# Kernel optimization log

Measured on AMD Instinct MI355X. Metric: run time of the kernel, lower is better.

## Reference

```python
import jax, jax.numpy as jnp
import numpy as np

N = 50000      # num nodes
E = 800000     # num edges (before self loops)
H = 2          # heads
C = 64         # out_channels (== in_dim, extra_layer=False)
L = 3          # n_layer
SLOPE = 0.2    # leaky_relu negative_slope


def setup_inputs() -> dict:
    key = jax.random.key(0)
    k1, k2, k3 = jax.random.split(key, 3)
    x = jax.random.normal(k1, (N, C), dtype=jnp.float32)
    edge_index = jax.random.randint(k2, (2, E), 0, N)
    att = jax.random.normal(k3, (L, H, C), dtype=jnp.float32) * 0.1  # glorot-ish scale
    bias = jnp.zeros((L, C), dtype=jnp.float32)
    return {"x": x, "edge_index": edge_index, "att": att, "bias": bias}


def _segment_softmax(alpha, dst, n):
    # alpha: [Etot, H], softmax over edges sharing the same destination node
    m = jax.ops.segment_max(alpha, dst, num_segments=n)          # [N, H]
    a = jnp.exp(alpha - m[dst])                                  # [Etot, H]
    s = jax.ops.segment_sum(a, dst, num_segments=n)              # [N, H]
    return a / (s[dst] + 1e-16)


def _gat_layer(x, src, dst, att_l, bias_l):
    # extra_layer=False: x_l == x_r == x broadcast over heads, so x_i + x_j is
    # head-independent; compute it once as [Etot, C].
    m = jax.nn.leaky_relu(x[dst] + x[src], negative_slope=SLOPE)  # [Etot, C]
    alpha = m @ att_l.T                                           # [Etot, H]
    alpha = _segment_softmax(alpha, dst, N)
    # message = x_j * alpha, scatter-add to destinations, then mean over heads
    outs = [jax.ops.segment_sum(x[src] * alpha[:, h:h + 1], dst, num_segments=N)
            for h in range(H)]                                    # H x [N, C]
    return jnp.stack(outs, 0).mean(0) + bias_l                    # [N, C]


def reference(x, edge_index, att, bias):
    # add self loops (add_self_loops=True)
    loops = jnp.arange(N, dtype=edge_index.dtype)
    src = jnp.concatenate([edge_index[0], loops])
    dst = jnp.concatenate([edge_index[1], loops])
    feats = [x]
    h = x
    for l in range(L):
        h = _gat_layer(h, src, dst, att[l], bias[l])
        feats.append(h)
    return jnp.stack(feats, axis=1).mean(axis=1)  # [N, C]
```

## Files before the change

### kernel.cpp

```cpp
#include <hip/hip_runtime.h>
#include <hip/hip_fp16.h>

#define NN 50000
#define EE 800000
#define CC 64
#define HH 2
#define LL 3
#define CAP 64
#define NB 782
#define BCAP 1280
#define CHUNK 8192
#define NBLK ((EE + CHUNK - 1) / CHUNK)



__global__ __launch_bounds__(1024) void k_bin(const int* __restrict__ ei,
                                              int* __restrict__ bcnt,
                                              unsigned int* __restrict__ bucket) {
    __shared__ unsigned int stash[CHUNK];
    __shared__ int hist[NB];
    __shared__ int rank[NB];
    __shared__ int base[NB];

    int c0 = blockIdx.x * CHUNK;
    int n = EE - c0; if (n > CHUNK) n = CHUNK;

    for (int b = threadIdx.x; b < NB; b += 1024) { hist[b] = 0; rank[b] = 0; }
    __syncthreads();

    for (int k = threadIdx.x; k < n; k += 1024) {
        unsigned int s = (unsigned int)ei[c0 + k];
        unsigned int d = (unsigned int)ei[EE + c0 + k];
        stash[k] = (d << 16) | s;
        atomicAdd(&hist[d >> 6], 1);
    }
    __syncthreads();

    for (int b = threadIdx.x; b < NB; b += 1024) {
        int c = hist[b];
        base[b] = c ? atomicAdd(&bcnt[b], c) : 0;
    }
    __syncthreads();

    for (int k = threadIdx.x; k < n; k += 1024) {
        unsigned int pk = stash[k];
        int b = (int)(pk >> 22);
        int r = atomicAdd(&rank[b], 1);
        int pos = base[b] + r;
        if (pos < BCAP) bucket[(size_t)b * BCAP + pos] = pk;
    }
}

__global__ __launch_bounds__(256) void k_place(const unsigned int* __restrict__ bucket,
                                               const int* __restrict__ bcnt,
                                               int* __restrict__ cnt,
                                               unsigned short* __restrict__ slots) {
    __shared__ int lcnt[64];
    int b = blockIdx.x;
    if (threadIdx.x < 64) lcnt[threadIdx.x] = 0;
    __syncthreads();
    int node0 = b << 6;
    int m = bcnt[b];
    if (m > BCAP) m = BCAP;
    const unsigned int* src = bucket + (size_t)b * BCAP;
    for (int i = threadIdx.x; i < m; i += 256) {
        unsigned int pk = src[i];
        int d = (int)(pk >> 16);
        int s = (int)(pk & 0xFFFFu);
        int pos = atomicAdd(&lcnt[d - node0], 1);
        if (pos < CAP) slots[(size_t)d * CAP + pos] = (unsigned short)s;
    }
    __syncthreads();
    if (threadIdx.x < 64) {
        int node = node0 + threadIdx.x;
        if (node < NN) cnt[node] = lcnt[threadIdx.x];
    }
}


typedef float v2f __attribute__((ext_vector_type(2)));

template <int CTRL>
__device__ __forceinline__ float dpp_add(float v) {
    int t = __builtin_amdgcn_update_dpp(0, __float_as_int(v), CTRL, 0xF, 0xF, true);
    return v + __int_as_float(t);
}

__device__ __forceinline__ float red16(float v) {
    v = dpp_add<0xB1>(v);
    v = dpp_add<0x4E>(v);
    v = dpp_add<0x141>(v);
    v = dpp_add<0x140>(v);
    return v;
}

__device__ __forceinline__ v2f lk2(v2f v) {
    v2f t = 0.2f * v;
    return __builtin_elementwise_max(v, t);
}

__device__ __forceinline__ v2f fma2(v2f a, v2f b, v2f c) {
    return __builtin_elementwise_fma(a, b, c);
}

template <bool F16>
__device__ __forceinline__ void ldrow(const char* hb, unsigned idx, unsigned q,
                                      v2f& lo, v2f& hi) {
    if constexpr (F16) {
        uint2 u = *(const uint2*)(hb + (idx << 7) + (q << 3));
        float2 fa = __half22float2(__builtin_bit_cast(__half2, u.x));
        float2 fb = __half22float2(__builtin_bit_cast(__half2, u.y));
        lo = (v2f){fa.x, fa.y}; hi = (v2f){fb.x, fb.y};
    } else {
        float4 v = *(const float4*)(hb + (idx << 8) + (q << 4));
        lo = (v2f){v.x, v.y}; hi = (v2f){v.z, v.w};
    }
}

template <bool FIRST, bool WRITE>
__global__ __launch_bounds__(256) void k_gat(const void* __restrict__ hin,
                                             const int* __restrict__ cnt,
                                             const unsigned short* __restrict__ slots,
                                             const float* __restrict__ att_l,
                                             const float* __restrict__ bias_l,
                                             void* __restrict__ hout,
                                             float* __restrict__ acc, int n) {
    constexpr bool F16IN = !FIRST;
    int wid = threadIdx.x >> 6;
    int lane = threadIdx.x & 63;
    int node = blockIdx.x * 4 + wid;
    if (node >= n) return;
    int sub = lane >> 4;
    unsigned q = (unsigned)(lane & 15);
    const char* hb = (const char*)hin;
    const v2f* attv = (const v2f*)att_l;
    v2f a0_01 = attv[2 * q],      a0_23 = attv[2 * q + 1];
    v2f a1_01 = attv[32 + 2 * q], a1_23 = attv[32 + 2 * q + 1];
    v2f hd01, hd23;
    ldrow<F16IN>(hb, (unsigned)node, q, hd01, hd23);
    int deg = cnt[node];
    if (deg > CAP) deg = CAP;
    const unsigned* rowu = (const unsigned*)(slots + (size_t)node * CAP);

    float s0, s1;
    v2f A0_01, A0_23, A1_01, A1_23;

    {
        v2f u01 = lk2(hd01 + hd01), u23 = lk2(hd23 + hd23);
        v2f d0 = fma2(u23, a0_23, u01 * a0_01);
        v2f d1 = fma2(u23, a1_23, u01 * a1_01);
        float p0 = red16(d0.x + d0.y);
        float p1 = red16(d1.x + d1.y);
        float e0 = 0.25f * __expf(p0), e1 = 0.25f * __expf(p1);
        s0 = e0; s1 = e1;
        A0_01 = e0 * hd01; A0_23 = e0 * hd23;
        A1_01 = e1 * hd01; A1_23 = e1 * hd23;
    }

    int npair = deg >> 1;
#pragma unroll 2
    for (int p = sub; p < npair; p += 4) {
        unsigned pk = rowu[p];
        v2f va01, va23, vb01, vb23;
        ldrow<F16IN>(hb, pk & 0xFFFFu, q, va01, va23);
        ldrow<F16IN>(hb, pk >> 16, q, vb01, vb23);
        v2f ma01 = lk2(va01 + hd01), ma23 = lk2(va23 + hd23);
        v2f mb01 = lk2(vb01 + hd01), mb23 = lk2(vb23 + hd23);
        v2f da0 = fma2(ma23, a0_23, ma01 * a0_01);
        v2f da1 = fma2(ma23, a1_23, ma01 * a1_01);
        v2f db0 = fma2(mb23, a0_23, mb01 * a0_01);
        v2f db1 = fma2(mb23, a1_23, mb01 * a1_01);
        float pa0 = red16(da0.x + da0.y);
        float pa1 = red16(da1.x + da1.y);
        float pb0 = red16(db0.x + db0.y);
        float pb1 = red16(db1.x + db1.y);
        float ea0 = __expf(pa0), ea1 = __expf(pa1);
        float eb0 = __expf(pb0), eb1 = __expf(pb1);
        s0 += ea0 + eb0;
        s1 += ea1 + eb1;
        v2f ea0v = {ea0, ea0}, ea1v = {ea1, ea1};
        v2f eb0v = {eb0, eb0}, eb1v = {eb1, eb1};
        A0_01 = fma2(ea0v, va01, fma2(eb0v, vb01, A0_01));
        A0_23 = fma2(ea0v, va23, fma2(eb0v, vb23, A0_23));
        A1_01 = fma2(ea1v, va01, fma2(eb1v, vb01, A1_01));
        A1_23 = fma2(ea1v, va23, fma2(eb1v, vb23, A1_23));
    }

    if (deg & 1) {
        int t = deg - 1;
        if (sub == ((t >> 1) & 3)) {
            unsigned s = ((const unsigned short*)rowu)[t];
            v2f hv01, hv23;
            ldrow<F16IN>(hb, s, q, hv01, hv23);
            v2f m01 = lk2(hv01 + hd01), m23 = lk2(hv23 + hd23);
            v2f d0 = fma2(m23, a0_23, m01 * a0_01);
            v2f d1 = fma2(m23, a1_23, m01 * a1_01);
            float p0 = red16(d0.x + d0.y);
            float p1 = red16(d1.x + d1.y);
            float e0 = __expf(p0), e1 = __expf(p1);
            s0 += e0; s1 += e1;
            v2f e0v = {e0, e0}, e1v = {e1, e1};
            A0_01 = fma2(e0v, hv01, A0_01); A0_23 = fma2(e0v, hv23, A0_23);
            A1_01 = fma2(e1v, hv01, A1_01); A1_23 = fma2(e1v, hv23, A1_23);
        }
    }

#pragma unroll
    for (int step = 16; step <= 32; step <<= 1) {
        s0 += __shfl_xor(s0, step);
        s1 += __shfl_xor(s1, step);
        A0_01.x += __shfl_xor(A0_01.x, step); A0_01.y += __shfl_xor(A0_01.y, step);
        A0_23.x += __shfl_xor(A0_23.x, step); A0_23.y += __shfl_xor(A0_23.y, step);
        A1_01.x += __shfl_xor(A1_01.x, step); A1_01.y += __shfl_xor(A1_01.y, step);
        A1_23.x += __shfl_xor(A1_23.x, step); A1_23.y += __shfl_xor(A1_23.y, step);
    }

    if (sub == 0) {
        float inv0 = 0.5f / (s0 + 1e-16f);
        float inv1 = 0.5f / (s1 + 1e-16f);
        float4 b4 = ((const float4*)bias_l)[q];
        v2f o01, o23;
        o01.x = A0_01.x * inv0 + A1_01.x * inv1 + b4.x;
        o01.y = A0_01.y * inv0 + A1_01.y * inv1 + b4.y;
        o23.x = A0_23.x * inv0 + A1_23.x * inv1 + b4.z;
        o23.y = A0_23.y * inv0 + A1_23.y * inv1 + b4.w;
        if constexpr (WRITE) {
            __half2 w0 = __float22half2_rn((float2){o01.x, o01.y});
            __half2 w1 = __float22half2_rn((float2){o23.x, o23.y});
            uint2 u = {__builtin_bit_cast(unsigned, w0),
                       __builtin_bit_cast(unsigned, w1)};
            *(uint2*)((char*)hout + ((size_t)node << 7) + (q << 3)) = u;
        }
        float4* accp = (float4*)acc + (size_t)node * 16 + q;
        float4 ac;
        if (FIRST) {
            ac.x = 0.25f * (hd01.x + o01.x); ac.y = 0.25f * (hd01.y + o01.y);
            ac.z = 0.25f * (hd23.x + o23.x); ac.w = 0.25f * (hd23.y + o23.y);
        } else {
            ac = *accp;
            ac.x += 0.25f * o01.x; ac.y += 0.25f * o01.y;
            ac.z += 0.25f * o23.x; ac.w += 0.25f * o23.y;
        }
        *accp = ac;
    }
}


static inline size_t align256(size_t x) { return (x + 255) & ~(size_t)255; }

extern "C" void kernel_launch(void* const* d_in, const int* in_sizes, int n_in,
                              void* d_out, int out_size, void* d_ws, size_t ws_size,
                              hipStream_t stream) {
    const float* x    = (const float*)d_in[0];
    const int*   ei   = (const int*)d_in[1];
    const float* att  = (const float*)d_in[2];
    const float* bias = (const float*)d_in[3];
    float* acc = (float*)d_out;

    char* w = (char*)d_ws;
    int* bcnt   = (int*)w;              w += align256((size_t)NB * sizeof(int));
    int* cnt    = (int*)w;              w += align256((size_t)NN * sizeof(int));
    unsigned int* bucket = (unsigned int*)w;
    w += align256((size_t)NB * BCAP * sizeof(unsigned int));
    unsigned short* slots = (unsigned short*)w;
    w += align256((size_t)NN * CAP * sizeof(unsigned short) + 256);
    void* hA16  = (void*)w;             w += align256((size_t)NN * CC * sizeof(__half));
    void* hB16  = (void*)w;             w += align256((size_t)NN * CC * sizeof(__half));

    const int B = 256;

    hipMemsetAsync(bcnt, 0, (size_t)NB * sizeof(int), stream);
    k_bin<<<NBLK, 1024, 0, stream>>>(ei, bcnt, bucket);
    k_place<<<NB, B, 0, stream>>>(bucket, bcnt, cnt, slots);

    k_gat<true, true><<<(NN + 3) / 4, B, 0, stream>>>(
        x, cnt, slots, att, bias, hA16, acc, NN);
    k_gat<false, true><<<(NN + 3) / 4, B, 0, stream>>>(
        hA16, cnt, slots, att + (size_t)HH * CC, bias + CC, hB16, acc, NN);
    k_gat<false, false><<<(NN + 3) / 4, B, 0, stream>>>(
        hB16, cnt, slots, att + (size_t)2 * HH * CC, bias + 2 * CC, nullptr, acc, NN);
}
```

Baseline: 193.0 us.

## Process two destination nodes per wavefront to raise memory-level parallelism

Each wavefront now handles two destination nodes at once, interleaving their edge loops so four neighbor-row gathers are in flight per iteration, and halves the grid size. Sub-group 0 writes node A and sub-group 1 writes node B. This is meant to hide gather latency and amortise per-wave setup such as the attention-vector loads. In exchange it raises register pressure, and the node with fewer edges does masked dummy loads from row 0 while the other finishes.

```diff
diff --git a/kernel.cpp b/kernel.cpp
--- a/kernel.cpp
+++ b/kernel.cpp
@@ -104,17 +104,66 @@
 }
 
 template <bool F16>
-__device__ __forceinline__ void ldrow(const char* hb, unsigned idx, unsigned q,
+__device__ __forceinline__ void ldrow(const char* hbq, unsigned idx,
                                       v2f& lo, v2f& hi) {
     if constexpr (F16) {
-        uint2 u = *(const uint2*)(hb + (idx << 7) + (q << 3));
+        uint2 u = *(const uint2*)(hbq + ((size_t)idx << 7));
         float2 fa = __half22float2(__builtin_bit_cast(__half2, u.x));
         float2 fb = __half22float2(__builtin_bit_cast(__half2, u.y));
         lo = (v2f){fa.x, fa.y}; hi = (v2f){fb.x, fb.y};
     } else {
-        float4 v = *(const float4*)(hb + (idx << 8) + (q << 4));
+        float4 v = *(const float4*)(hbq + ((size_t)idx << 8));
         lo = (v2f){v.x, v.y}; hi = (v2f){v.z, v.w};
     }
+}
+
+__device__ __forceinline__ void edge_pair(v2f va01, v2f va23, v2f vb01, v2f vb23,
+                                          v2f hd01, v2f hd23,
+                                          v2f a0_01, v2f a0_23,
+                                          v2f a1_01, v2f a1_23, bool act,
+                                          float& s0, float& s1,
+                                          v2f& A0_01, v2f& A0_23,
+                                          v2f& A1_01, v2f& A1_23) {
+    v2f ma01 = lk2(va01 + hd01), ma23 = lk2(va23 + hd23);
+    v2f mb01 = lk2(vb01 + hd01), mb23 = lk2(vb23 + hd23);
+    v2f da0 = fma2(ma23, a0_23, ma01 * a0_01);
+    v2f da1 = fma2(ma23, a1_23, ma01 * a1_01);
+    v2f db0 = fma2(mb23, a0_23, mb01 * a0_01);
+    v2f db1 = fma2(mb23, a1_23, mb01 * a1_01);
+    float pa0 = red16(da0.x + da0.y);
+    float pa1 = red16(da1.x + da1.y);
+    float pb0 = red16(db0.x + db0.y);
+    float pb1 = red16(db1.x + db1.y);
+    float ea0 = act ? __expf(pa0) : 0.f;
+    float ea1 = act ? __expf(pa1) : 0.f;
+    float eb0 = act ? __expf(pb0) : 0.f;
+    float eb1 = act ? __expf(pb1) : 0.f;
+    s0 += ea0 + eb0;
+    s1 += ea1 + eb1;
+    v2f ea0v = {ea0, ea0}, ea1v = {ea1, ea1};
+    v2f eb0v = {eb0, eb0}, eb1v = {eb1, eb1};
+    A0_01 = fma2(ea0v, va01, fma2(eb0v, vb01, A0_01));
+    A0_23 = fma2(ea0v, va23, fma2(eb0v, vb23, A0_23));
+    A1_01 = fma2(ea1v, va01, fma2(eb1v, vb01, A1_01));
+    A1_23 = fma2(ea1v, va23, fma2(eb1v, vb23, A1_23));
+}
+
+__device__ __forceinline__ void edge_one(v2f hv01, v2f hv23, v2f hd01, v2f hd23,
+                                         v2f a0_01, v2f a0_23,
+                                         v2f a1_01, v2f a1_23,
+                                         float& s0, float& s1,
+                                         v2f& A0_01, v2f& A0_23,
+                                         v2f& A1_01, v2f& A1_23) {
+    v2f m01 = lk2(hv01 + hd01), m23 = lk2(hv23 + hd23);
+    v2f d0 = fma2(m23, a0_23, m01 * a0_01);
+    v2f d1 = fma2(m23, a1_23, m01 * a1_01);
+    float p0 = red16(d0.x + d0.y);
+    float p1 = red16(d1.x + d1.y);
+    float e0 = __expf(p0), e1 = __expf(p1);
+    s0 += e0; s1 += e1;
+    v2f e0v = {e0, e0}, e1v = {e1, e1};
+    A0_01 = fma2(e0v, hv01, A0_01); A0_23 = fma2(e0v, hv23, A0_23);
+    A1_01 = fma2(e1v, hv01, A1_01); A1_23 = fma2(e1v, hv23, A1_23);
 }
 
 template <bool FIRST, bool WRITE>
@@ -128,94 +177,122 @@
     constexpr bool F16IN = !FIRST;
     int wid = threadIdx.x >> 6;
     int lane = threadIdx.x & 63;
-    int node = blockIdx.x * 4 + wid;
-    if (node >= n) return;
+    int nodeA = blockIdx.x * 8 + wid * 2;
+    if (nodeA >= n) return;
+    int nodeB = nodeA + 1;
+    bool vB = nodeB < n;
     int sub = lane >> 4;
     unsigned q = (unsigned)(lane & 15);
-    const char* hb = (const char*)hin;
+    const char* hbq = (const char*)hin + (q << (F16IN ? 3 : 4));
     const v2f* attv = (const v2f*)att_l;
     v2f a0_01 = attv[2 * q],      a0_23 = attv[2 * q + 1];
     v2f a1_01 = attv[32 + 2 * q], a1_23 = attv[32 + 2 * q + 1];
-    v2f hd01, hd23;
-    ldrow<F16IN>(hb, (unsigned)node, q, hd01, hd23);
-    int deg = cnt[node];
-    if (deg > CAP) deg = CAP;
-    const unsigned* rowu = (const unsigned*)(slots + (size_t)node * CAP);
-
-    float s0, s1;
-    v2f A0_01, A0_23, A1_01, A1_23;
+
+    v2f hdA01, hdA23, hdB01, hdB23;
+    ldrow<F16IN>(hbq, (unsigned)nodeA, hdA01, hdA23);
+    ldrow<F16IN>(hbq, (unsigned)(vB ? nodeB : nodeA), hdB01, hdB23);
+    int degA = cnt[nodeA];
+    if (degA > CAP) degA = CAP;
+    int degB = vB ? cnt[nodeB] : 0;
+    if (degB > CAP) degB = CAP;
+    const unsigned* rowuA = (const unsigned*)(slots + (size_t)nodeA * CAP);
+    const unsigned* rowuB = (const unsigned*)(slots + (size_t)nodeB * CAP);
+
+    float sA0, sA1, sB0, sB1;
+    v2f AA0_01, AA0_23, AA1_01, AA1_23;
+    v2f AB0_01, AB0_23, AB1_01, AB1_23;
 
     {
-        v2f u01 = lk2(hd01 + hd01), u23 = lk2(hd23 + hd23);
+        v2f u01 = lk2(hdA01 + hdA01), u23 = lk2(hdA23 + hdA23);
         v2f d0 = fma2(u23, a0_23, u01 * a0_01);
         v2f d1 = fma2(u23, a1_23, u01 * a1_01);
         float p0 = red16(d0.x + d0.y);
         float p1 = red16(d1.x + d1.y);
         float e0 = 0.25f * __expf(p0), e1 = 0.25f * __expf(p1);
-        s0 = e0; s1 = e1;
-        A0_01 = e0 * hd01; A0_23 = e0 * hd23;
-        A1_01 = e1 * hd01; A1_23 = e1 * hd23;
-    }
-
-    int npair = deg >> 1;
+        sA0 = e0; sA1 = e1;
+        AA0_01 = e0 * hdA01; AA0_23 = e0 * hdA23;
+        AA1_01 = e1 * hdA01; AA1_23 = e1 * hdA23;
+    }
+    {
+        v2f u01 = lk2(hdB01 + hdB01), u23 = lk2(hdB23 + hdB23);
+        v2f d0 = fma2(u23, a0_23, u01 * a0_01);
+        v2f d1 = fma2(u23, a1_23, u01 * a1_01);
+        float p0 = red16(d0.x + d0.y);
+        float p1 = red16(d1.x + d1.y);
+        float e0 = 0.25f * __expf(p0), e1 = 0.25f * __expf(p1);
+        sB0 = e0; sB1 = e1;
+        AB0_01 = e0 * hdB01; AB0_23 = e0 * hdB23;
+        AB1_01 = e1 * hdB01; AB1_23 = e1 * hdB23;
+    }
+
+    int npA = degA >> 1, npB = degB >> 1;
+    int tA = (npA > sub) ? ((npA - sub + 3) >> 2) : 0;
+    int tB = (npB > sub) ? ((npB - sub + 3) >> 2) : 0;
+    int tm = tA > tB ? tA : tB;
+    int pA = sub, pB = sub;
 #pragma unroll 2
-    for (int p = sub; p < npair; p += 4) {
-        unsigned pk = rowu[p];
-        v2f va01, va23, vb01, vb23;
-        ldrow<F16IN>(hb, pk & 0xFFFFu, q, va01, va23);
-        ldrow<F16IN>(hb, pk >> 16, q, vb01, vb23);
-        v2f ma01 = lk2(va01 + hd01), ma23 = lk2(va23 + hd23);
-        v2f mb01 = lk2(vb01 + hd01), mb23 = lk2(vb23 + hd23);
-        v2f da0 = fma2(ma23, a0_23, ma01 * a0_01);
-        v2f da1 = fma2(ma23, a1_23, ma01 * a1_01);
-        v2f db0 = fma2(mb23, a0_23, mb01 * a0_01);
-        v2f db1 = fma2(mb23, a1_23, mb01 * a1_01);
-        float pa0 = red16(da0.x + da0.y);
-        float pa1 = red16(da1.x + da1.y);
-        float pb0 = red16(db0.x + db0.y);
-        float pb1 = red16(db1.x + db1.y);
-        float ea0 = __expf(pa0), ea1 = __expf(pa1);
-        float eb0 = __expf(pb0), eb1 = __expf(pb1);
-        s0 += ea0 + eb0;
-        s1 += ea1 + eb1;
-        v2f ea0v = {ea0, ea0}, ea1v = {ea1, ea1};
-        v2f eb0v = {eb0, eb0}, eb1v = {eb1, eb1};
-        A0_01 = fma2(ea0v, va01, fma2(eb0v, vb01, A0_01));
-        A0_23 = fma2(ea0v, va23, fma2(eb0v, vb23, A0_23));
-        A1_01 = fma2(ea1v, va01, fma2(eb1v, vb01, A1_01));
-        A1_23 = fma2(ea1v, va23, fma2(eb1v, vb23, A1_23));
-    }
-
-    if (deg & 1) {
-        int t = deg - 1;
+    for (int i = 0; i < tm; ++i, pA += 4, pB += 4) {
+        bool aA = i < tA, aB = i < tB;
+        unsigned pkA = aA ? rowuA[pA] : 0u;
+        unsigned pkB = aB ? rowuB[pB] : 0u;
+        v2f vaA01, vaA23, vbA01, vbA23, vaB01, vaB23, vbB01, vbB23;
+        ldrow<F16IN>(hbq, pkA & 0xFFFFu, vaA01, vaA23);
+        ldrow<F16IN>(hbq, pkA >> 16,     vbA01, vbA23);
+        ldrow<F16IN>(hbq, pkB & 0xFFFFu, vaB01, vaB23);
+        ldrow<F16IN>(hbq, pkB >> 16,     vbB01, vbB23);
+        edge_pair(vaA01, vaA23, vbA01, vbA23, hdA01, hdA23,
+                  a0_01, a0_23, a1_01, a1_23, aA,
+                  sA0, sA1, AA0_01, AA0_23, AA1_01, AA1_23);
+        edge_pair(vaB01, vaB23, vbB01, vbB23, hdB01, hdB23,
+                  a0_01, a0_23, a1_01, a1_23, aB,
+                  sB0, sB1, AB0_01, AB0_23, AB1_01, AB1_23);
+    }
+
+    if (degA & 1) {
+        int t = degA - 1;
         if (sub == ((t >> 1) & 3)) {
-            unsigned s = ((const unsigned short*)rowu)[t];
+            unsigned s = ((const unsigned short*)rowuA)[t];
             v2f hv01, hv23;
-            ldrow<F16IN>(hb, s, q, hv01, hv23);
-            v2f m01 = lk2(hv01 + hd01), m23 = lk2(hv23 + hd23);
-            v2f d0 = fma2(m23, a0_23, m01 * a0_01);
-            v2f d1 = fma2(m23, a1_23, m01 * a1_01);
-            float p0 = red16(d0.x + d0.y);
-            float p1 = red16(d1.x + d1.y);
-            float e0 = __expf(p0), e1 = __expf(p1);
-            s0 += e0; s1 += e1;
-            v2f e0v = {e0, e0}, e1v = {e1, e1};
-            A0_01 = fma2(e0v, hv01, A0_01); A0_23 = fma2(e0v, hv23, A0_23);
-            A1_01 = fma2(e1v, hv01, A1_01); A1_23 = fma2(e1v, hv23, A1_23);
+            ldrow<F16IN>(hbq, s, hv01, hv23);
+            edge_one(hv01, hv23, hdA01, hdA23, a0_01, a0_23, a1_01, a1_23,
+                     sA0, sA1, AA0_01, AA0_23, AA1_01, AA1_23);
+        }
+    }
+    if (degB & 1) {
+        int t = degB - 1;
+        if (sub == ((t >> 1) & 3)) {
+            unsigned s = ((const unsigned short*)rowuB)[t];
+            v2f hv01, hv23;
+            ldrow<F16IN>(hbq, s, hv01, hv23);
+            edge_one(hv01, hv23, hdB01, hdB23, a0_01, a0_23, a1_01, a1_23,
+                     sB0, sB1, AB0_01, AB0_23, AB1_01, AB1_23);
         }
     }
 
 #pragma unroll
     for (int step = 16; step <= 32; step <<= 1) {
-        s0 += __shfl_xor(s0, step);
-        s1 += __shfl_xor(s1, step);
-        A0_01.x += __shfl_xor(A0_01.x, step); A0_01.y += __shfl_xor(A0_01.y, step);
-        A0_23.x += __shfl_xor(A0_23.x, step); A0_23.y += __shfl_xor(A0_23.y, step);
-        A1_01.x += __shfl_xor(A1_01.x, step); A1_01.y += __shfl_xor(A1_01.y, step);
-        A1_23.x += __shfl_xor(A1_23.x, step); A1_23.y += __shfl_xor(A1_23.y, step);
-    }
-
-    if (sub == 0) {
+        sA0 += __shfl_xor(sA0, step); sA1 += __shfl_xor(sA1, step);
+        sB0 += __shfl_xor(sB0, step); sB1 += __shfl_xor(sB1, step);
+        AA0_01.x += __shfl_xor(AA0_01.x, step); AA0_01.y += __shfl_xor(AA0_01.y, step);
+        AA0_23.x += __shfl_xor(AA0_23.x, step); AA0_23.y += __shfl_xor(AA0_23.y, step);
+        AA1_01.x += __shfl_xor(AA1_01.x, step); AA1_01.y += __shfl_xor(AA1_01.y, step);
+        AA1_23.x += __shfl_xor(AA1_23.x, step); AA1_23.y += __shfl_xor(AA1_23.y, step);
+        AB0_01.x += __shfl_xor(AB0_01.x, step); AB0_01.y += __shfl_xor(AB0_01.y, step);
+        AB0_23.x += __shfl_xor(AB0_23.x, step); AB0_23.y += __shfl_xor(AB0_23.y, step);
+        AB1_01.x += __shfl_xor(AB1_01.x, step); AB1_01.y += __shfl_xor(AB1_01.y, step);
+        AB1_23.x += __shfl_xor(AB1_23.x, step); AB1_23.y += __shfl_xor(AB1_23.y, step);
+    }
+
+    if (sub == 0 || (sub == 1 && vB)) {
+        int node = (sub == 0) ? nodeA : nodeB;
+        float s0 = (sub == 0) ? sA0 : sB0;
+        float s1 = (sub == 0) ? sA1 : sB1;
+        v2f A0_01 = (sub == 0) ? AA0_01 : AB0_01;
+        v2f A0_23 = (sub == 0) ? AA0_23 : AB0_23;
+        v2f A1_01 = (sub == 0) ? AA1_01 : AB1_01;
+        v2f A1_23 = (sub == 0) ? AA1_23 : AB1_23;
+        v2f hd01 = (sub == 0) ? hdA01 : hdB01;
+        v2f hd23 = (sub == 0) ? hdA23 : hdB23;
         float inv0 = 0.5f / (s0 + 1e-16f);
         float inv1 = 0.5f / (s1 + 1e-16f);
         float4 b4 = ((const float4*)bias_l)[q];
@@ -268,15 +345,16 @@
     void* hB16  = (void*)w;             w += align256((size_t)NN * CC * sizeof(__half));
 
     const int B = 256;
+    const int GG = (NN + 7) / 8;
 
     hipMemsetAsync(bcnt, 0, (size_t)NB * sizeof(int), stream);
     k_bin<<<NBLK, 1024, 0, stream>>>(ei, bcnt, bucket);
     k_place<<<NB, B, 0, stream>>>(bucket, bcnt, cnt, slots);
 
-    k_gat<true, true><<<(NN + 3) / 4, B, 0, stream>>>(
+    k_gat<true, true><<<GG, B, 0, stream>>>(
         x, cnt, slots, att, bias, hA16, acc, NN);
-    k_gat<false, true><<<(NN + 3) / 4, B, 0, stream>>>(
+    k_gat<false, true><<<GG, B, 0, stream>>>(
         hA16, cnt, slots, att + (size_t)HH * CC, bias + CC, hB16, acc, NN);
-    k_gat<false, false><<<(NN + 3) / 4, B, 0, stream>>>(
+    k_gat<false, false><<<GG, B, 0, stream>>>(
         hB16, cnt, slots, att + (size_t)2 * HH * CC, bias + 2 * CC, nullptr, acc, NN);
 }
```

New measurement: 202.3 us. 4.8% more time.
